# Optimization experiments

Hardware: AMD Instinct MI355X
Metric: run time of the kernel (lower is better)

## Reference

```python
import jax, jax.numpy as jnp
import numpy as np

N, E, DIN, H, DOUT, NBLK = 50000, 300000, 963, 256, 3, 6


def gconv(x, src, dst, ew, W, Wl, b):
    # support = x @ W ; out[i] = sum_j ew_ij * support[j] + x[i] @ W_loop + b
    sup = x @ W
    agg = jax.ops.segment_sum(ew[:, None] * sup[src], dst, num_segments=N)
    return agg + x @ Wl + b


def setup_inputs() -> dict:
    key = jax.random.key(0)
    ks = jax.random.split(key, 16)
    s = 0.05
    x = jax.random.normal(ks[0], (N, DIN), jnp.float32)
    src = jax.random.randint(ks[1], (E,), 0, N, dtype=jnp.int32)
    dst = jax.random.randint(ks[2], (E,), 0, N, dtype=jnp.int32)
    ew = jax.random.uniform(ks[3], (E,), jnp.float32)
    W1 = jax.random.normal(ks[4], (DIN, H), jnp.float32) * s
    Wl1 = jax.random.normal(ks[5], (DIN, H), jnp.float32) * s
    b1 = jnp.zeros((H,), jnp.float32)
    # stacked residual-block weights: [NBLK, 2 convs, H, H]
    blkW = jax.random.normal(ks[6], (NBLK, 2, H, H), jnp.float32) * s
    blkWl = jax.random.normal(ks[7], (NBLK, 2, H, H), jnp.float32) * s
    blkb = jnp.zeros((NBLK, 2, H), jnp.float32)
    W2 = jax.random.normal(ks[8], (H, DOUT), jnp.float32) * s
    Wl2 = jax.random.normal(ks[9], (H, DOUT), jnp.float32) * s
    b2 = jnp.zeros((DOUT,), jnp.float32)
    return dict(x=x, src=src, dst=dst, ew=ew, W1=W1, Wl1=Wl1, b1=b1,
                blkW=blkW, blkWl=blkWl, blkb=blkb, W2=W2, Wl2=Wl2, b2=b2)


def reference(x, src, dst, ew, W1, Wl1, b1, blkW, blkWl, blkb, W2, Wl2, b2):
    h = jax.nn.relu(gconv(x, src, dst, ew, W1, Wl1, b1))

    def block(h, p):
        W, Wl, b = p  # W: [2,H,H]
        y = jax.nn.relu(gconv(h, src, dst, ew, W[0], Wl[0], b[0]))
        y = jax.nn.relu(gconv(y, src, dst, ew, W[1], Wl[1], b[1]))
        return (h + y) * 0.5, None

    x_hidden, _ = jax.lax.scan(block, h, (blkW, blkWl, blkb))
    x_out = gconv(x_hidden, src, dst, ew, W2, Wl2, b2)
    return (x_out, x_hidden)
```

## Files before the change

kernel.cpp:

```cpp
#include <hip/hip_runtime.h>

typedef __attribute__((ext_vector_type(8))) short short8;
typedef __attribute__((ext_vector_type(4))) float f32x4;
typedef __attribute__((ext_vector_type(4), aligned(4))) float f32x4u;

constexpr int kN = 50000;
constexpr int kE = 300000;
constexpr int kDIN = 963;
constexpr int kH = 256;
constexpr int kNBLK = 6;

__device__ inline unsigned short f2bf(float f) {
    unsigned u = __float_as_uint(f);
    u = u + 0x7FFFu + ((u >> 16) & 1u);
    return (unsigned short)(u >> 16);
}
__device__ inline float bf2f(unsigned short s) {
    return __uint_as_float(((unsigned)s) << 16);
}

__device__ inline void gload_lds16(const void* g, void* l) {
    __builtin_amdgcn_global_load_lds(
        (const __attribute__((address_space(1))) void*)g,
        (__attribute__((address_space(3))) void*)l, 16, 0, 0);
}

__global__ __launch_bounds__(512) void gemm_l1(
    const float* __restrict__ Av, const unsigned short* __restrict__ Bt,
    const float* __restrict__ bias,
    unsigned short* __restrict__ supb, unsigned short* __restrict__ tpreb,
    int M, int Kpad, int Kvalid, int Astride)
{
    __shared__ __align__(16) char smem[49152];
    char* As = smem;
    char* Bs = smem + 16384;

    const int tid = threadIdx.x;
    const int wid = tid >> 6;
    const int lane = tid & 63;
    const int wr = wid >> 2, wc = wid & 3;

    const int nwg = gridDim.x;
    const int q = nwg >> 3, r = nwg & 7;
    const int xcd = blockIdx.x & 7, idx = blockIdx.x >> 3;
    const int t = (xcd < r ? xcd * (q + 1) : r * (q + 1) + (xcd - r) * q) + idx;
    const int r0 = (t >> 1) * 128;
    const int c0 = (t & 1) * 256;

    f32x4 acc[4][4];
#pragma unroll
    for (int i = 0; i < 4; ++i)
#pragma unroll
        for (int j = 0; j < 4; ++j) acc[i][j] = f32x4{0.f, 0.f, 0.f, 0.f};

    const int l_row = lane >> 3;
    const int l_c   = lane & 7;

    for (int k0 = 0; k0 < Kpad; k0 += 64) {
#pragma unroll
        for (int p = 0; p < 4; ++p) {
            int row = wid * 32 + p * 8 + l_row;
            int csw = l_c ^ (row & 7);
            const unsigned short* g = Bt + (long)(c0 + row) * Kpad + k0 + csw * 8;
            gload_lds16(g, Bs + (wid * 32 + p * 8) * 128);
        }
        {
            const int row = tid >> 2;
            const int kq = tid & 3;
            int grow = r0 + row; if (grow >= M) grow = M - 1;
            const float* ar = Av + (long)grow * Astride;
#pragma unroll
            for (int j = 0; j < 2; ++j) {
                int k16 = kq * 2 + j;
                int kb = k0 + k16 * 8;
                short8 v;
                if (kb + 8 <= Kvalid) {
                    f32x4u f0 = *(const f32x4u*)(ar + kb);
                    f32x4u f1 = *(const f32x4u*)(ar + kb + 4);
#pragma unroll
                    for (int ii = 0; ii < 4; ++ii) {
                        v[ii]     = (short)f2bf(f0[ii]);
                        v[ii + 4] = (short)f2bf(f1[ii]);
                    }
                } else {
#pragma unroll
                    for (int ii = 0; ii < 8; ++ii) {
                        int k = kb + ii;
                        float f = (k < Kvalid) ? ar[k] : 0.f;
                        v[ii] = (short)f2bf(f);
                    }
                }
                *(short8*)(As + row * 128 + ((k16 ^ (row & 7)) << 4)) = v;
            }
        }
        __syncthreads();
#pragma unroll
        for (int kk = 0; kk < 2; ++kk) {
            short8 af[4], bfr[4];
            const int kg = kk * 4 + (lane >> 4);
#pragma unroll
            for (int nr = 0; nr < 4; ++nr) {
                int row = wr * 64 + nr * 16 + (lane & 15);
                af[nr] = *(const short8*)(As + row * 128 + ((kg ^ (row & 7)) << 4));
            }
#pragma unroll
            for (int mc = 0; mc < 4; ++mc) {
                int row = wc * 64 + mc * 16 + (lane & 15);
                bfr[mc] = *(const short8*)(Bs + row * 128 + ((kg ^ (row & 7)) << 4));
            }
#pragma unroll
            for (int mc = 0; mc < 4; ++mc)
#pragma unroll
                for (int nr = 0; nr < 4; ++nr)
                    acc[mc][nr] = __builtin_amdgcn_mfma_f32_16x16x32_bf16(
                        bfr[mc], af[nr], acc[mc][nr], 0, 0, 0);
        }
        __syncthreads();
    }

    const bool isSup = (c0 == 0);
    unsigned short* outp = isSup ? supb : tpreb;
    float* eL = (float*)smem;
    const int wrow = wr * 16 + (lane & 15);
    const int qc = (lane >> 4) << 2;

    for (int nr = 0; nr < 4; ++nr) {
        __syncthreads();
#pragma unroll
        for (int mc = 0; mc < 4; ++mc) {
            const int col = wc * 64 + mc * 16 + qc;
            f32x4 v = acc[mc][nr];
            if (!isSup) v += *(const f32x4*)(bias + col);
            const int c16 = col >> 2;
            *(f32x4*)(eL + wrow * 256 + ((c16 ^ wrow) << 2)) = v;
        }
        __syncthreads();
        const int tr = tid >> 4, j = tid & 15;
        const int gr = r0 + (tr >> 4) * 64 + nr * 16 + (tr & 15);
        if (gr < M) {
#pragma unroll
            for (int p = 0; p < 2; ++p) {
                const int u = j + 16 * p;
                f32x4 lo = *(const f32x4*)(eL + tr * 256 + (((2 * u) ^ tr) << 2));
                f32x4 hi = *(const f32x4*)(eL + tr * 256 + (((2 * u + 1) ^ tr) << 2));
                uint4 pk;
                pk.x = (unsigned)f2bf(lo[0]) | ((unsigned)f2bf(lo[1]) << 16);
                pk.y = (unsigned)f2bf(lo[2]) | ((unsigned)f2bf(lo[3]) << 16);
                pk.z = (unsigned)f2bf(hi[0]) | ((unsigned)f2bf(hi[1]) << 16);
                pk.w = (unsigned)f2bf(hi[2]) | ((unsigned)f2bf(hi[3]) << 16);
                *(uint4*)(outp + (long)gr * 256 + u * 8) = pk;
            }
        }
    }
}

template<int RES>
__global__ __launch_bounds__(256) void gemm_blk(
    const unsigned short* __restrict__ act, const unsigned short* __restrict__ xagg,
    const unsigned short* __restrict__ Bt, const float* __restrict__ bias,
    const unsigned short* __restrict__ hbf_res,
    unsigned short* __restrict__ outbf, float* __restrict__ hf32)
{
    __shared__ __align__(16) char smem[32768];
    char* As = smem;
    char* Bs = smem + 16384;

    const int tid = threadIdx.x;
    const int wid = tid >> 6;
    const int lane = tid & 63;
    const int wr = wid >> 1, wc = wid & 1;

    const int nwg = gridDim.x;
    const int q = nwg >> 3, r = nwg & 7;
    const int xcd = blockIdx.x & 7, idx = blockIdx.x >> 3;
    const int t = (xcd < r ? xcd * (q + 1) : r * (q + 1) + (xcd - r) * q) + idx;
    const int r0 = (t >> 1) * 128;
    const int c0 = (t & 1) * 128;

    f32x4 acc[4][4];
#pragma unroll
    for (int i = 0; i < 4; ++i)
#pragma unroll
        for (int j = 0; j < 4; ++j) acc[i][j] = f32x4{0.f, 0.f, 0.f, 0.f};

    const int l_row = lane >> 3;
    const int l_c   = lane & 7;

    for (int k0 = 0; k0 < 512; k0 += 64) {
#pragma unroll
        for (int p = 0; p < 4; ++p) {
            int row = wid * 32 + p * 8 + l_row;
            int csw = l_c ^ (row & 7);
            const unsigned short* g = Bt + (long)(c0 + row) * 512 + k0 + csw * 8;
            gload_lds16(g, Bs + (wid * 32 + p * 8) * 128);
        }
        const unsigned short* Asrc = (k0 < 256) ? (act + k0) : (xagg + (k0 - 256));
#pragma unroll
        for (int p = 0; p < 4; ++p) {
            int row = wid * 32 + p * 8 + l_row;
            int grow = r0 + row; if (grow >= kN) grow = kN - 1;
            int csw = l_c ^ (row & 7);
            const unsigned short* g = Asrc + (long)grow * 256 + csw * 8;
            gload_lds16(g, As + (wid * 32 + p * 8) * 128);
        }
        __syncthreads();
#pragma unroll
        for (int kk = 0; kk < 2; ++kk) {
            short8 af[4], bfr[4];
            const int kg = kk * 4 + (lane >> 4);
#pragma unroll
            for (int nr = 0; nr < 4; ++nr) {
                int row = wr * 64 + nr * 16 + (lane & 15);
                af[nr] = *(const short8*)(As + row * 128 + ((kg ^ (row & 7)) << 4));
            }
#pragma unroll
            for (int mc = 0; mc < 4; ++mc) {
                int row = wc * 64 + mc * 16 + (lane & 15);
                bfr[mc] = *(const short8*)(Bs + row * 128 + ((kg ^ (row & 7)) << 4));
            }
#pragma unroll
            for (int mc = 0; mc < 4; ++mc)
#pragma unroll
                for (int nr = 0; nr < 4; ++nr)
                    acc[mc][nr] = __builtin_amdgcn_mfma_f32_16x16x32_bf16(
                        bfr[mc], af[nr], acc[mc][nr], 0, 0, 0);
        }
        __syncthreads();
    }

    float* eL = (float*)smem;
    const int wrow = wr * 16 + (lane & 15);
    const int qc = (lane >> 4) << 2;

    for (int nr = 0; nr < 4; ++nr) {
        __syncthreads();
#pragma unroll
        for (int mc = 0; mc < 4; ++mc) {
            const int col = wc * 64 + mc * 16 + qc;
            f32x4 v = acc[mc][nr] + *(const f32x4*)(bias + c0 + col);
            const int c16 = col >> 2;
            *(f32x4*)(eL + wrow * 128 + ((c16 ^ wrow) << 2)) = v;
        }
        __syncthreads();
        const int tr = tid >> 3, j = tid & 7;
        const int gr = r0 + (tr >> 4) * 64 + nr * 16 + (tr & 15);
        if (gr < kN) {
#pragma unroll
            for (int p = 0; p < 2; ++p) {
                const int u = j + 8 * p;
                f32x4 lo = *(const f32x4*)(eL + tr * 128 + (((2 * u) ^ tr) << 2));
                f32x4 hi = *(const f32x4*)(eL + tr * 128 + (((2 * u + 1) ^ tr) << 2));
#pragma unroll
                for (int ii = 0; ii < 4; ++ii) {
                    lo[ii] = fmaxf(lo[ii], 0.f);
                    hi[ii] = fmaxf(hi[ii], 0.f);
                }
                const long gcol = (long)gr * 256 + c0 + u * 8;
                if (RES >= 1) {
                    uint4 hv = *(const uint4*)(hbf_res + gcol);
                    lo[0] = (bf2f((unsigned short)(hv.x & 0xFFFF)) + lo[0]) * 0.5f;
                    lo[1] = (bf2f((unsigned short)(hv.x >> 16))    + lo[1]) * 0.5f;
                    lo[2] = (bf2f((unsigned short)(hv.y & 0xFFFF)) + lo[2]) * 0.5f;
                    lo[3] = (bf2f((unsigned short)(hv.y >> 16))    + lo[3]) * 0.5f;
                    hi[0] = (bf2f((unsigned short)(hv.z & 0xFFFF)) + hi[0]) * 0.5f;
                    hi[1] = (bf2f((unsigned short)(hv.z >> 16))    + hi[1]) * 0.5f;
                    hi[2] = (bf2f((unsigned short)(hv.w & 0xFFFF)) + hi[2]) * 0.5f;
                    hi[3] = (bf2f((unsigned short)(hv.w >> 16))    + hi[3]) * 0.5f;
                }
                if (RES == 2) {
                    *(f32x4*)(hf32 + gcol)     = lo;
                    *(f32x4*)(hf32 + gcol + 4) = hi;
                }
                uint4 pk;
                pk.x = (unsigned)f2bf(lo[0]) | ((unsigned)f2bf(lo[1]) << 16);
                pk.y = (unsigned)f2bf(lo[2]) | ((unsigned)f2bf(lo[3]) << 16);
                pk.z = (unsigned)f2bf(hi[0]) | ((unsigned)f2bf(hi[1]) << 16);
                pk.w = (unsigned)f2bf(hi[2]) | ((unsigned)f2bf(hi[3]) << 16);
                *(uint4*)(outbf + gcol) = pk;
            }
        }
    }
}

template<int MODE>
__global__ __launch_bounds__(256) void agg16_kernel(
    const unsigned short* __restrict__ srcbuf, const unsigned short* __restrict__ tpreb,
    const int* __restrict__ rowptr, const int* __restrict__ e_src,
    const float* __restrict__ e_w, unsigned short* __restrict__ outb)
{
    const int tid = threadIdx.x;
    const int sub = tid >> 5;
    const int l   = tid & 31;
    const long node = (long)blockIdx.x * 8 + sub;
    if (node >= kN) return;
    const int c0 = l * 8;

    f32x4 a0 = {0.f, 0.f, 0.f, 0.f}, a1 = {0.f, 0.f, 0.f, 0.f};
    if (MODE == 1) {
        uint4 tv = *(const uint4*)(tpreb + node * 256 + c0);
        a0[0] = bf2f((unsigned short)(tv.x & 0xFFFF)); a0[1] = bf2f((unsigned short)(tv.x >> 16));
        a0[2] = bf2f((unsigned short)(tv.y & 0xFFFF)); a0[3] = bf2f((unsigned short)(tv.y >> 16));
        a1[0] = bf2f((unsigned short)(tv.z & 0xFFFF)); a1[1] = bf2f((unsigned short)(tv.z >> 16));
        a1[2] = bf2f((unsigned short)(tv.w & 0xFFFF)); a1[3] = bf2f((unsigned short)(tv.w >> 16));
    }

    int b = rowptr[node];
    const int e = rowptr[node + 1];

#define ACC16(V, W) \
    a0[0] += (W) * bf2f((unsigned short)((V).x & 0xFFFF)); \
    a0[1] += (W) * bf2f((unsigned short)((V).x >> 16));    \
    a0[2] += (W) * bf2f((unsigned short)((V).y & 0xFFFF)); \
    a0[3] += (W) * bf2f((unsigned short)((V).y >> 16));    \
    a1[0] += (W) * bf2f((unsigned short)((V).z & 0xFFFF)); \
    a1[1] += (W) * bf2f((unsigned short)((V).z >> 16));    \
    a1[2] += (W) * bf2f((unsigned short)((V).w & 0xFFFF)); \
    a1[3] += (W) * bf2f((unsigned short)((V).w >> 16));

    for (; b + 4 <= e; b += 4) {
        const int s0 = e_src[b],     s1 = e_src[b + 1];
        const int s2 = e_src[b + 2], s3 = e_src[b + 3];
        const float w0 = e_w[b],     w1 = e_w[b + 1];
        const float w2 = e_w[b + 2], w3 = e_w[b + 3];
        uint4 v0 = *(const uint4*)(srcbuf + (long)s0 * 256 + c0);
        uint4 v1 = *(const uint4*)(srcbuf + (long)s1 * 256 + c0);
        uint4 v2 = *(const uint4*)(srcbuf + (long)s2 * 256 + c0);
        uint4 v3 = *(const uint4*)(srcbuf + (long)s3 * 256 + c0);
        ACC16(v0, w0) ACC16(v1, w1) ACC16(v2, w2) ACC16(v3, w3)
    }
    for (; b < e; ++b) {
        const int s = e_src[b];
        const float w = e_w[b];
        uint4 v = *(const uint4*)(srcbuf + (long)s * 256 + c0);
        ACC16(v, w)
    }
#undef ACC16

    if (MODE == 1) {
#pragma unroll
        for (int ii = 0; ii < 4; ++ii) {
            a0[ii] = fmaxf(a0[ii], 0.f);
            a1[ii] = fmaxf(a1[ii], 0.f);
        }
    }
    uint4 pk;
    pk.x = (unsigned)f2bf(a0[0]) | ((unsigned)f2bf(a0[1]) << 16);
    pk.y = (unsigned)f2bf(a0[2]) | ((unsigned)f2bf(a0[3]) << 16);
    pk.z = (unsigned)f2bf(a1[0]) | ((unsigned)f2bf(a1[1]) << 16);
    pk.w = (unsigned)f2bf(a1[2]) | ((unsigned)f2bf(a1[3]) << 16);
    *(uint4*)(outb + node * 256 + c0) = pk;
}

__global__ __launch_bounds__(256) void cvt_w1_kernel(
    const float* __restrict__ W1, const float* __restrict__ Wl1,
    unsigned short* __restrict__ out)
{
    int idx = blockIdx.x * 256 + threadIdx.x;
    if (idx >= 512 * 1024) return;
    int c = idx >> 10, k = idx & 1023;
    float v = 0.f;
    if (k < kDIN) v = (c < 256) ? W1[(long)k * 256 + c] : Wl1[(long)k * 256 + (c - 256)];
    out[idx] = f2bf(v);
}

__global__ __launch_bounds__(256) void cvt_blk_kernel(
    const float* __restrict__ blkW, const float* __restrict__ blkWl,
    unsigned short* __restrict__ out)
{
    int idx = blockIdx.x * 256 + threadIdx.x;
    if (idx >= 12 * 256 * 512) return;
    int l = idx >> 17;
    int rem = idx & 131071;
    int c = rem >> 9, k = rem & 511;
    float v = (k < 256) ? blkWl[((long)l * 256 + k) * 256 + c]
                        : blkW[((long)l * 256 + (k - 256)) * 256 + c];
    out[idx] = f2bf(v);
}

__global__ __launch_bounds__(256) void hist_kernel(const int* __restrict__ dst,
                                                   int* __restrict__ counts)
{
    int e = blockIdx.x * 256 + threadIdx.x;
    if (e < kE) atomicAdd(&counts[dst[e]], 1);
}

__global__ __launch_bounds__(1024) void scan1_kernel(
    const int* __restrict__ counts, int* __restrict__ rowptr, int* __restrict__ bsum)
{
    __shared__ int s[1024];
    const int tid = threadIdx.x;
    const int g = blockIdx.x * 1024 + tid;
    const int v = (g < kN) ? counts[g] : 0;
    s[tid] = v; __syncthreads();
    for (int off = 1; off < 1024; off <<= 1) {
        int tv = (tid >= off) ? s[tid - off] : 0;
        __syncthreads();
        s[tid] += tv;
        __syncthreads();
    }
    if (g < kN) rowptr[g] = s[tid] - v;
    if (tid == 1023) bsum[blockIdx.x] = s[1023];
}

__global__ __launch_bounds__(64) void scan2_kernel(int* __restrict__ bsum, int nb)
{
    __shared__ int s[64];
    const int tid = threadIdx.x;
    const int v = (tid < nb) ? bsum[tid] : 0;
    s[tid] = v; __syncthreads();
    for (int off = 1; off < 64; off <<= 1) {
        int tv = (tid >= off) ? s[tid - off] : 0;
        __syncthreads();
        s[tid] += tv;
        __syncthreads();
    }
    if (tid < nb) bsum[tid] = s[tid] - v;
}

__global__ __launch_bounds__(256) void scan3_kernel(
    int* __restrict__ rowptr, const int* __restrict__ bsum, int* __restrict__ cursor)
{
    int g = blockIdx.x * 256 + threadIdx.x;
    if (g < kN) {
        int r = rowptr[g] + bsum[g >> 10];
        rowptr[g] = r;
        cursor[g] = r;
    }
    if (g == 0) rowptr[kN] = kE;
}

__global__ __launch_bounds__(256) void fill_kernel(
    const int* __restrict__ src, const int* __restrict__ dst,
    const float* __restrict__ ew, int* __restrict__ cursor,
    int* __restrict__ e_src, float* __restrict__ e_w)
{
    int e = blockIdx.x * 256 + threadIdx.x;
    if (e >= kE) return;
    int d = dst[e];
    int pos = atomicAdd(&cursor[d], 1);
    e_src[pos] = src[e];
    e_w[pos] = ew[e];
}

__global__ __launch_bounds__(64) void final_layer_kernel(
    const unsigned short* __restrict__ hbf, const float* __restrict__ W2,
    const float* __restrict__ Wl2, const float* __restrict__ b2,
    float* __restrict__ sup2, float* __restrict__ x_out)
{
    const int row = blockIdx.x;
    const int lane = threadIdx.x;
    const unsigned short* hr = hbf + (long)row * kH;
    float accW[3] = {0.f, 0.f, 0.f};
    float accL[3] = {0.f, 0.f, 0.f};
#pragma unroll
    for (int kb = 0; kb < kH / 64; ++kb) {
        int k = kb * 64 + lane;
        float v = bf2f(hr[k]);
#pragma unroll
        for (int c = 0; c < 3; ++c) {
            accW[c] = fmaf(v, W2[k * 3 + c], accW[c]);
            accL[c] = fmaf(v, Wl2[k * 3 + c], accL[c]);
        }
    }
#pragma unroll
    for (int off = 32; off > 0; off >>= 1) {
#pragma unroll
        for (int c = 0; c < 3; ++c) {
            accW[c] += __shfl_down(accW[c], off);
            accL[c] += __shfl_down(accL[c], off);
        }
    }
    if (lane == 0) {
#pragma unroll
        for (int c = 0; c < 3; ++c) {
            sup2[row * 3 + c] = accW[c];
            x_out[row * 3 + c] = accL[c] + b2[c];
        }
    }
}

__global__ __launch_bounds__(256) void scatter3_kernel(
    const float* __restrict__ sup2, const int* __restrict__ src,
    const int* __restrict__ dst, const float* __restrict__ ew,
    float* __restrict__ x_out)
{
    int e = blockIdx.x * 256 + threadIdx.x;
    if (e >= kE) return;
    int s = src[e];
    int d = dst[e];
    float w = ew[e];
#pragma unroll
    for (int c = 0; c < 3; ++c)
        atomicAdd(&x_out[(long)d * 3 + c], w * sup2[(long)s * 3 + c]);
}

extern "C" void kernel_launch(void* const* d_in, const int* in_sizes, int n_in,
                              void* d_out, int out_size, void* d_ws, size_t ws_size,
                              hipStream_t stream)
{
    const float* x    = (const float*)d_in[0];
    const int*   src  = (const int*)d_in[1];
    const int*   dst  = (const int*)d_in[2];
    const float* ew   = (const float*)d_in[3];
    const float* W1   = (const float*)d_in[4];
    const float* Wl1  = (const float*)d_in[5];
    const float* b1   = (const float*)d_in[6];
    const float* blkW  = (const float*)d_in[7];
    const float* blkWl = (const float*)d_in[8];
    const float* blkb  = (const float*)d_in[9];
    const float* W2   = (const float*)d_in[10];
    const float* Wl2  = (const float*)d_in[11];
    const float* b2   = (const float*)d_in[12];

    float* out   = (float*)d_out;
    float* x_out = out;
    float* h     = out + (long)kN * 3;

    char* w = (char*)d_ws;
    size_t off = 0;
    auto carve = [&](size_t bytes) { char* p = w + off; off = (off + bytes + 255) & ~(size_t)255; return p; };
    unsigned short* supb  = (unsigned short*)carve(12800000UL * 2);
    unsigned short* tpreb = (unsigned short*)carve(12800000UL * 2);
    unsigned short* tact  = (unsigned short*)carve(12800000UL * 2);
    unsigned short* hbf   = (unsigned short*)carve(12800000UL * 2);
    unsigned short* w1c   = (unsigned short*)carve(512UL * 1024 * 2);
    unsigned short* blkc  = (unsigned short*)carve(12UL * 256 * 512 * 2);
    int*   e_src  = (int*)carve(kE * 4);
    float* e_w    = (float*)carve(kE * 4);
    int*   counts = (int*)carve(50176 * 4);
    int*   rowptr = (int*)carve(50176 * 4);
    int*   cursor = (int*)carve(50176 * 4);
    int*   bsum   = (int*)carve(64 * 4);
    float* sup2   = (float*)carve((long)kN * 3 * 4);
    unsigned short* xagg = tpreb;

    hipMemsetAsync(counts, 0, 50176 * 4, stream);
    hist_kernel<<<(kE + 255) / 256, 256, 0, stream>>>(dst, counts);
    scan1_kernel<<<49, 1024, 0, stream>>>(counts, rowptr, bsum);
    scan2_kernel<<<1, 64, 0, stream>>>(bsum, 49);
    scan3_kernel<<<(kN + 255) / 256, 256, 0, stream>>>(rowptr, bsum, cursor);
    fill_kernel<<<(kE + 255) / 256, 256, 0, stream>>>(src, dst, ew, cursor, e_src, e_w);

    cvt_w1_kernel<<<2048, 256, 0, stream>>>(W1, Wl1, w1c);
    cvt_blk_kernel<<<6144, 256, 0, stream>>>(blkW, blkWl, blkc);

    const int l1_grid  = 2 * ((kN + 127) / 128);
    const int blk_grid = 2 * ((kN + 127) / 128);
    const int agg_grid = (kN + 7) / 8;

    gemm_l1<<<l1_grid, 512, 0, stream>>>(x, w1c, b1, supb, tpreb,
                                         kN, 1024, kDIN, kDIN);
    agg16_kernel<1><<<agg_grid, 256, 0, stream>>>(supb, tpreb, rowptr, e_src, e_w, hbf);

    for (int l = 0; l < 2 * kNBLK; ++l) {
        const unsigned short* act_in = (l & 1) ? tact : hbf;
        unsigned short* act_out      = (l & 1) ? hbf : tact;
        agg16_kernel<0><<<agg_grid, 256, 0, stream>>>(act_in, nullptr, rowptr, e_src, e_w, xagg);
        const unsigned short* B = blkc + (long)l * 256 * 512;
        const float* bb = blkb + (long)l * 256;
        if (l & 1) {
            if (l == 2 * kNBLK - 1)
                gemm_blk<2><<<blk_grid, 256, 0, stream>>>(act_in, xagg, B, bb, hbf, act_out, h);
            else
                gemm_blk<1><<<blk_grid, 256, 0, stream>>>(act_in, xagg, B, bb, hbf, act_out, nullptr);
        } else {
            gemm_blk<0><<<blk_grid, 256, 0, stream>>>(act_in, xagg, B, bb, nullptr, act_out, nullptr);
        }
    }

    final_layer_kernel<<<kN, 64, 0, stream>>>(hbf, W2, Wl2, b2, sup2, x_out);
    scatter3_kernel<<<(kE + 255) / 256, 256, 0, stream>>>(sup2, src, dst, ew, x_out);
}
```

Measured before the change: 961.7 us.

## Fuse neighbor aggregation into block GEMM A-tile loading

Drops the separate aggregation kernel for the 12 residual-block convs and builds the aggregated half of the A tile (K 256..511) inside the GEMM. Each thread gathers its neighbors' bf16 rows for a 16-column slice per K-step and writes the packed result into swizzled LDS. The tile becomes 64 rows by the full 256 output columns, so each block computes its aggregation once, and the intermediate xagg buffer write and read go away. In exchange, the gather is a serial per-edge loop with scattered global loads inside the GEMM K-loop, which stalls MFMA work and cannot be prefetched. Each row's CSR edge list is also re-read for every aggregated K-step.

```diff
diff --git a/kernel.cpp b/kernel.cpp
--- a/kernel.cpp
+++ b/kernel.cpp
@@ -156,26 +156,26 @@
 
 template<int RES>
 __global__ __launch_bounds__(256) void gemm_blk(
-    const unsigned short* __restrict__ act, const unsigned short* __restrict__ xagg,
+    const unsigned short* __restrict__ act,
     const unsigned short* __restrict__ Bt, const float* __restrict__ bias,
+    const int* __restrict__ rowptr, const int* __restrict__ e_src,
+    const float* __restrict__ e_w,
     const unsigned short* __restrict__ hbf_res,
     unsigned short* __restrict__ outbf, float* __restrict__ hf32)
 {
-    __shared__ __align__(16) char smem[32768];
+    __shared__ __align__(16) char smem[40960];
     char* As = smem;
-    char* Bs = smem + 16384;
+    char* Bs = smem + 8192;
 
     const int tid = threadIdx.x;
     const int wid = tid >> 6;
     const int lane = tid & 63;
-    const int wr = wid >> 1, wc = wid & 1;
 
     const int nwg = gridDim.x;
     const int q = nwg >> 3, r = nwg & 7;
     const int xcd = blockIdx.x & 7, idx = blockIdx.x >> 3;
     const int t = (xcd < r ? xcd * (q + 1) : r * (q + 1) + (xcd - r) * q) + idx;
-    const int r0 = (t >> 1) * 128;
-    const int c0 = (t & 1) * 128;
+    const int r0 = t * 64;
 
     f32x4 acc[4][4];
 #pragma unroll
@@ -186,22 +186,67 @@
     const int l_row = lane >> 3;
     const int l_c   = lane & 7;
 
+    const int g_row  = tid >> 2;
+    const int g_quad = tid & 3;
+    int g_grow = r0 + g_row; if (g_grow >= kN) g_grow = kN - 1;
+    const int g_beg = rowptr[g_grow];
+    const int g_end = rowptr[g_grow + 1];
+
     for (int k0 = 0; k0 < 512; k0 += 64) {
 #pragma unroll
-        for (int p = 0; p < 4; ++p) {
-            int row = wid * 32 + p * 8 + l_row;
+        for (int p = 0; p < 8; ++p) {
+            int row = wid * 64 + p * 8 + l_row;
             int csw = l_c ^ (row & 7);
-            const unsigned short* g = Bt + (long)(c0 + row) * 512 + k0 + csw * 8;
-            gload_lds16(g, Bs + (wid * 32 + p * 8) * 128);
-        }
-        const unsigned short* Asrc = (k0 < 256) ? (act + k0) : (xagg + (k0 - 256));
-#pragma unroll
-        for (int p = 0; p < 4; ++p) {
-            int row = wid * 32 + p * 8 + l_row;
-            int grow = r0 + row; if (grow >= kN) grow = kN - 1;
-            int csw = l_c ^ (row & 7);
-            const unsigned short* g = Asrc + (long)grow * 256 + csw * 8;
-            gload_lds16(g, As + (wid * 32 + p * 8) * 128);
+            const unsigned short* g = Bt + (long)row * 512 + k0 + csw * 8;
+            gload_lds16(g, Bs + (wid * 64 + p * 8) * 128);
+        }
+        if (k0 < 256) {
+#pragma unroll
+            for (int p = 0; p < 2; ++p) {
+                int row = wid * 16 + p * 8 + l_row;
+                int grow = r0 + row; if (grow >= kN) grow = kN - 1;
+                int csw = l_c ^ (row & 7);
+                const unsigned short* g = act + (long)grow * 256 + k0 + csw * 8;
+                gload_lds16(g, As + (wid * 16 + p * 8) * 128);
+            }
+        } else {
+            const int cbase = (k0 - 256) + g_quad * 16;
+            f32x4 g0 = {0.f,0.f,0.f,0.f}, g1 = {0.f,0.f,0.f,0.f};
+            f32x4 g2 = {0.f,0.f,0.f,0.f}, g3 = {0.f,0.f,0.f,0.f};
+            for (int b = g_beg; b < g_end; ++b) {
+                const int s = e_src[b];
+                const float w = e_w[b];
+                const unsigned short* ap = act + (long)s * 256 + cbase;
+                uint4 v0 = *(const uint4*)(ap);
+                uint4 v1 = *(const uint4*)(ap + 8);
+                g0[0] += w * bf2f((unsigned short)(v0.x & 0xFFFF));
+                g0[1] += w * bf2f((unsigned short)(v0.x >> 16));
+                g0[2] += w * bf2f((unsigned short)(v0.y & 0xFFFF));
+                g0[3] += w * bf2f((unsigned short)(v0.y >> 16));
+                g1[0] += w * bf2f((unsigned short)(v0.z & 0xFFFF));
+                g1[1] += w * bf2f((unsigned short)(v0.z >> 16));
+                g1[2] += w * bf2f((unsigned short)(v0.w & 0xFFFF));
+                g1[3] += w * bf2f((unsigned short)(v0.w >> 16));
+                g2[0] += w * bf2f((unsigned short)(v1.x & 0xFFFF));
+                g2[1] += w * bf2f((unsigned short)(v1.x >> 16));
+                g2[2] += w * bf2f((unsigned short)(v1.y & 0xFFFF));
+                g2[3] += w * bf2f((unsigned short)(v1.y >> 16));
+                g3[0] += w * bf2f((unsigned short)(v1.z & 0xFFFF));
+                g3[1] += w * bf2f((unsigned short)(v1.z >> 16));
+                g3[2] += w * bf2f((unsigned short)(v1.w & 0xFFFF));
+                g3[3] += w * bf2f((unsigned short)(v1.w >> 16));
+            }
+            short8 o0, o1;
+#pragma unroll
+            for (int ii = 0; ii < 4; ++ii) {
+                o0[ii]     = (short)f2bf(g0[ii]);
+                o0[ii + 4] = (short)f2bf(g1[ii]);
+                o1[ii]     = (short)f2bf(g2[ii]);
+                o1[ii + 4] = (short)f2bf(g3[ii]);
+            }
+            const int ch = g_quad * 2;
+            *(short8*)(As + g_row * 128 + ((ch       ^ (g_row & 7)) << 4)) = o0;
+            *(short8*)(As + g_row * 128 + (((ch + 1) ^ (g_row & 7)) << 4)) = o1;
         }
         __syncthreads();
 #pragma unroll
@@ -210,12 +255,12 @@
             const int kg = kk * 4 + (lane >> 4);
 #pragma unroll
             for (int nr = 0; nr < 4; ++nr) {
-                int row = wr * 64 + nr * 16 + (lane & 15);
+                int row = nr * 16 + (lane & 15);
                 af[nr] = *(const short8*)(As + row * 128 + ((kg ^ (row & 7)) << 4));
             }
 #pragma unroll
             for (int mc = 0; mc < 4; ++mc) {
-                int row = wc * 64 + mc * 16 + (lane & 15);
+                int row = wid * 64 + mc * 16 + (lane & 15);
                 bfr[mc] = *(const short8*)(Bs + row * 128 + ((kg ^ (row & 7)) << 4));
             }
 #pragma unroll
@@ -229,33 +274,33 @@
     }
 
     float* eL = (float*)smem;
-    const int wrow = wr * 16 + (lane & 15);
+    const int row16 = lane & 15;
     const int qc = (lane >> 4) << 2;
 
     for (int nr = 0; nr < 4; ++nr) {
         __syncthreads();
 #pragma unroll
         for (int mc = 0; mc < 4; ++mc) {
-            const int col = wc * 64 + mc * 16 + qc;
-            f32x4 v = acc[mc][nr] + *(const f32x4*)(bias + c0 + col);
+            const int col = wid * 64 + mc * 16 + qc;
+            f32x4 v = acc[mc][nr] + *(const f32x4*)(bias + col);
             const int c16 = col >> 2;
-            *(f32x4*)(eL + wrow * 128 + ((c16 ^ wrow) << 2)) = v;
-        }
-        __syncthreads();
-        const int tr = tid >> 3, j = tid & 7;
-        const int gr = r0 + (tr >> 4) * 64 + nr * 16 + (tr & 15);
+            *(f32x4*)(eL + row16 * 256 + ((c16 ^ row16) << 2)) = v;
+        }
+        __syncthreads();
+        const int tr = tid >> 4, j = tid & 15;
+        const int gr = r0 + nr * 16 + tr;
         if (gr < kN) {
 #pragma unroll
             for (int p = 0; p < 2; ++p) {
-                const int u = j + 8 * p;
-                f32x4 lo = *(const f32x4*)(eL + tr * 128 + (((2 * u) ^ tr) << 2));
-                f32x4 hi = *(const f32x4*)(eL + tr * 128 + (((2 * u + 1) ^ tr) << 2));
+                const int u = j + 16 * p;
+                f32x4 lo = *(const f32x4*)(eL + tr * 256 + (((2 * u) ^ tr) << 2));
+                f32x4 hi = *(const f32x4*)(eL + tr * 256 + (((2 * u + 1) ^ tr) << 2));
 #pragma unroll
                 for (int ii = 0; ii < 4; ++ii) {
                     lo[ii] = fmaxf(lo[ii], 0.f);
                     hi[ii] = fmaxf(hi[ii], 0.f);
                 }
-                const long gcol = (long)gr * 256 + c0 + u * 8;
+                const long gcol = (long)gr * 256 + u * 8;
                 if (RES >= 1) {
                     uint4 hv = *(const uint4*)(hbf_res + gcol);
                     lo[0] = (bf2f((unsigned short)(hv.x & 0xFFFF)) + lo[0]) * 0.5f;
@@ -282,9 +327,8 @@
     }
 }
 
-template<int MODE>
-__global__ __launch_bounds__(256) void agg16_kernel(
-    const unsigned short* __restrict__ srcbuf, const unsigned short* __restrict__ tpreb,
+__global__ __launch_bounds__(256) void agg_l1_kernel(
+    const unsigned short* __restrict__ supb, const unsigned short* __restrict__ tpreb,
     const int* __restrict__ rowptr, const int* __restrict__ e_src,
     const float* __restrict__ e_w, unsigned short* __restrict__ outb)
 {
@@ -295,14 +339,12 @@
     if (node >= kN) return;
     const int c0 = l * 8;
 
-    f32x4 a0 = {0.f, 0.f, 0.f, 0.f}, a1 = {0.f, 0.f, 0.f, 0.f};
-    if (MODE == 1) {
-        uint4 tv = *(const uint4*)(tpreb + node * 256 + c0);
-        a0[0] = bf2f((unsigned short)(tv.x & 0xFFFF)); a0[1] = bf2f((unsigned short)(tv.x >> 16));
-        a0[2] = bf2f((unsigned short)(tv.y & 0xFFFF)); a0[3] = bf2f((unsigned short)(tv.y >> 16));
-        a1[0] = bf2f((unsigned short)(tv.z & 0xFFFF)); a1[1] = bf2f((unsigned short)(tv.z >> 16));
-        a1[2] = bf2f((unsigned short)(tv.w & 0xFFFF)); a1[3] = bf2f((unsigned short)(tv.w >> 16));
-    }
+    uint4 tv = *(const uint4*)(tpreb + node * 256 + c0);
+    f32x4 a0, a1;
+    a0[0] = bf2f((unsigned short)(tv.x & 0xFFFF)); a0[1] = bf2f((unsigned short)(tv.x >> 16));
+    a0[2] = bf2f((unsigned short)(tv.y & 0xFFFF)); a0[3] = bf2f((unsigned short)(tv.y >> 16));
+    a1[0] = bf2f((unsigned short)(tv.z & 0xFFFF)); a1[1] = bf2f((unsigned short)(tv.z >> 16));
+    a1[2] = bf2f((unsigned short)(tv.w & 0xFFFF)); a1[3] = bf2f((unsigned short)(tv.w >> 16));
 
     int b = rowptr[node];
     const int e = rowptr[node + 1];
@@ -322,26 +364,24 @@
         const int s2 = e_src[b + 2], s3 = e_src[b + 3];
         const float w0 = e_w[b],     w1 = e_w[b + 1];
         const float w2 = e_w[b + 2], w3 = e_w[b + 3];
-        uint4 v0 = *(const uint4*)(srcbuf + (long)s0 * 256 + c0);
-        uint4 v1 = *(const uint4*)(srcbuf + (long)s1 * 256 + c0);
-        uint4 v2 = *(const uint4*)(srcbuf + (long)s2 * 256 + c0);
-        uint4 v3 = *(const uint4*)(srcbuf + (long)s3 * 256 + c0);
+        uint4 v0 = *(const uint4*)(supb + (long)s0 * 256 + c0);
+        uint4 v1 = *(const uint4*)(supb + (long)s1 * 256 + c0);
+        uint4 v2 = *(const uint4*)(supb + (long)s2 * 256 + c0);
+        uint4 v3 = *(const uint4*)(supb + (long)s3 * 256 + c0);
         ACC16(v0, w0) ACC16(v1, w1) ACC16(v2, w2) ACC16(v3, w3)
     }
     for (; b < e; ++b) {
         const int s = e_src[b];
         const float w = e_w[b];
-        uint4 v = *(const uint4*)(srcbuf + (long)s * 256 + c0);
+        uint4 v = *(const uint4*)(supb + (long)s * 256 + c0);
         ACC16(v, w)
     }
 #undef ACC16
 
-    if (MODE == 1) {
-#pragma unroll
-        for (int ii = 0; ii < 4; ++ii) {
-            a0[ii] = fmaxf(a0[ii], 0.f);
-            a1[ii] = fmaxf(a1[ii], 0.f);
-        }
+#pragma unroll
+    for (int ii = 0; ii < 4; ++ii) {
+        a0[ii] = fmaxf(a0[ii], 0.f);
+        a1[ii] = fmaxf(a1[ii], 0.f);
     }
     uint4 pk;
     pk.x = (unsigned)f2bf(a0[0]) | ((unsigned)f2bf(a0[1]) << 16);
@@ -532,7 +572,6 @@
     int*   cursor = (int*)carve(50176 * 4);
     int*   bsum   = (int*)carve(64 * 4);
     float* sup2   = (float*)carve((long)kN * 3 * 4);
-    unsigned short* xagg = tpreb;
 
     hipMemsetAsync(counts, 0, 50176 * 4, stream);
     hist_kernel<<<(kE + 255) / 256, 256, 0, stream>>>(dst, counts);
@@ -545,26 +584,28 @@
     cvt_blk_kernel<<<6144, 256, 0, stream>>>(blkW, blkWl, blkc);
 
     const int l1_grid  = 2 * ((kN + 127) / 128);
-    const int blk_grid = 2 * ((kN + 127) / 128);
+    const int blk_grid = (kN + 63) / 64;
     const int agg_grid = (kN + 7) / 8;
 
     gemm_l1<<<l1_grid, 512, 0, stream>>>(x, w1c, b1, supb, tpreb,
                                          kN, 1024, kDIN, kDIN);
-    agg16_kernel<1><<<agg_grid, 256, 0, stream>>>(supb, tpreb, rowptr, e_src, e_w, hbf);
+    agg_l1_kernel<<<agg_grid, 256, 0, stream>>>(supb, tpreb, rowptr, e_src, e_w, hbf);
 
     for (int l = 0; l < 2 * kNBLK; ++l) {
         const unsigned short* act_in = (l & 1) ? tact : hbf;
         unsigned short* act_out      = (l & 1) ? hbf : tact;
-        agg16_kernel<0><<<agg_grid, 256, 0, stream>>>(act_in, nullptr, rowptr, e_src, e_w, xagg);
         const unsigned short* B = blkc + (long)l * 256 * 512;
         const float* bb = blkb + (long)l * 256;
         if (l & 1) {
             if (l == 2 * kNBLK - 1)
-                gemm_blk<2><<<blk_grid, 256, 0, stream>>>(act_in, xagg, B, bb, hbf, act_out, h);
+                gemm_blk<2><<<blk_grid, 256, 0, stream>>>(
+                    act_in, B, bb, rowptr, e_src, e_w, hbf, act_out, h);
             else
-                gemm_blk<1><<<blk_grid, 256, 0, stream>>>(act_in, xagg, B, bb, hbf, act_out, nullptr);
+                gemm_blk<1><<<blk_grid, 256, 0, stream>>>(
+                    act_in, B, bb, rowptr, e_src, e_w, hbf, act_out, nullptr);
         } else {
-            gemm_blk<0><<<blk_grid, 256, 0, stream>>>(act_in, xagg, B, bb, nullptr, act_out, nullptr);
+            gemm_blk<0><<<blk_grid, 256, 0, stream>>>(
+                act_in, B, bb, rowptr, e_src, e_w, nullptr, act_out, nullptr);
         }
     }
 
```

Result: slower. 1.417 ms (+47.3%).

## Compute both output halves per block in first-layer GEMM to reuse A tile

Applied to the files above, without the earlier changes.

The first-layer GEMM now has each workgroup compute all 512 output columns (support and self-loop parts) for its 128-row tile instead of splitting them across two workgroups. The fp32 input x is therefore loaded and converted to bf16 once rather than twice, halving the main memory read of the 50000x963 input. In exchange, LDS use grows to 80 KB and accumulators double to 128 floats per thread, which lowers occupancy and raises register pressure, and the grid is halved.

```diff
diff --git a/kernel.cpp b/kernel.cpp
--- a/kernel.cpp
+++ b/kernel.cpp
@@ -31,9 +31,10 @@
     unsigned short* __restrict__ supb, unsigned short* __restrict__ tpreb,
     int M, int Kpad, int Kvalid, int Astride)
 {
-    __shared__ __align__(16) char smem[49152];
-    char* As = smem;
-    char* Bs = smem + 16384;
+    __shared__ __align__(16) char smem[81920];
+    char* As  = smem;
+    char* Bs0 = smem + 16384;
+    char* Bs1 = smem + 49152;
 
     const int tid = threadIdx.x;
     const int wid = tid >> 6;
@@ -44,14 +45,15 @@
     const int q = nwg >> 3, r = nwg & 7;
     const int xcd = blockIdx.x & 7, idx = blockIdx.x >> 3;
     const int t = (xcd < r ? xcd * (q + 1) : r * (q + 1) + (xcd - r) * q) + idx;
-    const int r0 = (t >> 1) * 128;
-    const int c0 = (t & 1) * 256;
-
-    f32x4 acc[4][4];
-#pragma unroll
-    for (int i = 0; i < 4; ++i)
-#pragma unroll
-        for (int j = 0; j < 4; ++j) acc[i][j] = f32x4{0.f, 0.f, 0.f, 0.f};
+    const int r0 = t * 128;
+
+    f32x4 acc[2][4][4];
+#pragma unroll
+    for (int hf = 0; hf < 2; ++hf)
+#pragma unroll
+        for (int i = 0; i < 4; ++i)
+#pragma unroll
+            for (int j = 0; j < 4; ++j) acc[hf][i][j] = f32x4{0.f, 0.f, 0.f, 0.f};
 
     const int l_row = lane >> 3;
     const int l_c   = lane & 7;
@@ -61,8 +63,10 @@
         for (int p = 0; p < 4; ++p) {
             int row = wid * 32 + p * 8 + l_row;
             int csw = l_c ^ (row & 7);
-            const unsigned short* g = Bt + (long)(c0 + row) * Kpad + k0 + csw * 8;
-            gload_lds16(g, Bs + (wid * 32 + p * 8) * 128);
+            const unsigned short* g0 = Bt + (long)row * Kpad + k0 + csw * 8;
+            gload_lds16(g0, Bs0 + (wid * 32 + p * 8) * 128);
+            const unsigned short* g1 = Bt + (long)(256 + row) * Kpad + k0 + csw * 8;
+            gload_lds16(g1, Bs1 + (wid * 32 + p * 8) * 128);
         }
         {
             const int row = tid >> 2;
@@ -96,59 +100,66 @@
         __syncthreads();
 #pragma unroll
         for (int kk = 0; kk < 2; ++kk) {
-            short8 af[4], bfr[4];
             const int kg = kk * 4 + (lane >> 4);
+            short8 af[4];
 #pragma unroll
             for (int nr = 0; nr < 4; ++nr) {
                 int row = wr * 64 + nr * 16 + (lane & 15);
                 af[nr] = *(const short8*)(As + row * 128 + ((kg ^ (row & 7)) << 4));
             }
 #pragma unroll
-            for (int mc = 0; mc < 4; ++mc) {
-                int row = wc * 64 + mc * 16 + (lane & 15);
-                bfr[mc] = *(const short8*)(Bs + row * 128 + ((kg ^ (row & 7)) << 4));
-            }
-#pragma unroll
-            for (int mc = 0; mc < 4; ++mc)
-#pragma unroll
-                for (int nr = 0; nr < 4; ++nr)
-                    acc[mc][nr] = __builtin_amdgcn_mfma_f32_16x16x32_bf16(
-                        bfr[mc], af[nr], acc[mc][nr], 0, 0, 0);
-        }
-        __syncthreads();
-    }
-
-    const bool isSup = (c0 == 0);
-    unsigned short* outp = isSup ? supb : tpreb;
+            for (int hf = 0; hf < 2; ++hf) {
+                const char* Bs = hf ? Bs1 : Bs0;
+                short8 bfr[4];
+#pragma unroll
+                for (int mc = 0; mc < 4; ++mc) {
+                    int row = wc * 64 + mc * 16 + (lane & 15);
+                    bfr[mc] = *(const short8*)(Bs + row * 128 + ((kg ^ (row & 7)) << 4));
+                }
+#pragma unroll
+                for (int mc = 0; mc < 4; ++mc)
+#pragma unroll
+                    for (int nr = 0; nr < 4; ++nr)
+                        acc[hf][mc][nr] = __builtin_amdgcn_mfma_f32_16x16x32_bf16(
+                            bfr[mc], af[nr], acc[hf][mc][nr], 0, 0, 0);
+            }
+        }
+        __syncthreads();
+    }
+
     float* eL = (float*)smem;
     const int wrow = wr * 16 + (lane & 15);
     const int qc = (lane >> 4) << 2;
 
-    for (int nr = 0; nr < 4; ++nr) {
-        __syncthreads();
-#pragma unroll
-        for (int mc = 0; mc < 4; ++mc) {
-            const int col = wc * 64 + mc * 16 + qc;
-            f32x4 v = acc[mc][nr];
-            if (!isSup) v += *(const f32x4*)(bias + col);
-            const int c16 = col >> 2;
-            *(f32x4*)(eL + wrow * 256 + ((c16 ^ wrow) << 2)) = v;
-        }
-        __syncthreads();
-        const int tr = tid >> 4, j = tid & 15;
-        const int gr = r0 + (tr >> 4) * 64 + nr * 16 + (tr & 15);
-        if (gr < M) {
-#pragma unroll
-            for (int p = 0; p < 2; ++p) {
-                const int u = j + 16 * p;
-                f32x4 lo = *(const f32x4*)(eL + tr * 256 + (((2 * u) ^ tr) << 2));
-                f32x4 hi = *(const f32x4*)(eL + tr * 256 + (((2 * u + 1) ^ tr) << 2));
-                uint4 pk;
-                pk.x = (unsigned)f2bf(lo[0]) | ((unsigned)f2bf(lo[1]) << 16);
-                pk.y = (unsigned)f2bf(lo[2]) | ((unsigned)f2bf(lo[3]) << 16);
-                pk.z = (unsigned)f2bf(hi[0]) | ((unsigned)f2bf(hi[1]) << 16);
-                pk.w = (unsigned)f2bf(hi[2]) | ((unsigned)f2bf(hi[3]) << 16);
-                *(uint4*)(outp + (long)gr * 256 + u * 8) = pk;
+#pragma unroll
+    for (int hf = 0; hf < 2; ++hf) {
+        unsigned short* outp = hf ? tpreb : supb;
+        for (int nr = 0; nr < 4; ++nr) {
+            __syncthreads();
+#pragma unroll
+            for (int mc = 0; mc < 4; ++mc) {
+                const int col = wc * 64 + mc * 16 + qc;
+                f32x4 v = acc[hf][mc][nr];
+                if (hf) v += *(const f32x4*)(bias + col);
+                const int c16 = col >> 2;
+                *(f32x4*)(eL + wrow * 256 + ((c16 ^ wrow) << 2)) = v;
+            }
+            __syncthreads();
+            const int tr = tid >> 4, j = tid & 15;
+            const int gr = r0 + (tr >> 4) * 64 + nr * 16 + (tr & 15);
+            if (gr < M) {
+#pragma unroll
+                for (int p = 0; p < 2; ++p) {
+                    const int u = j + 16 * p;
+                    f32x4 lo = *(const f32x4*)(eL + tr * 256 + (((2 * u) ^ tr) << 2));
+                    f32x4 hi = *(const f32x4*)(eL + tr * 256 + (((2 * u + 1) ^ tr) << 2));
+                    uint4 pk;
+                    pk.x = (unsigned)f2bf(lo[0]) | ((unsigned)f2bf(lo[1]) << 16);
+                    pk.y = (unsigned)f2bf(lo[2]) | ((unsigned)f2bf(lo[3]) << 16);
+                    pk.z = (unsigned)f2bf(hi[0]) | ((unsigned)f2bf(hi[1]) << 16);
+                    pk.w = (unsigned)f2bf(hi[2]) | ((unsigned)f2bf(hi[3]) << 16);
+                    *(uint4*)(outp + (long)gr * 256 + u * 8) = pk;
+                }
             }
         }
     }
@@ -544,7 +555,7 @@
     cvt_w1_kernel<<<2048, 256, 0, stream>>>(W1, Wl1, w1c);
     cvt_blk_kernel<<<6144, 256, 0, stream>>>(blkW, blkWl, blkc);
 
-    const int l1_grid  = 2 * ((kN + 127) / 128);
+    const int l1_grid  = (kN + 127) / 128;
     const int blk_grid = 2 * ((kN + 127) / 128);
     const int agg_grid = (kN + 7) / 8;
 
```

New measurement: 955.1 us (median of 2 runs). No clear change (-0.7%).
